# Optimization experiments

Hardware: AMD Instinct MI355X
Metric: run time of the kernel (lower is better)

The kernel has to match this reference:

```python
import jax, jax.numpy as jnp
import numpy as np

B, H, W, C, A, K = 1_000_000, 4, 4, 3, 4, 20
# slicing offsets (w_offset, h_offset) exactly as in the torch code
OFFSETS = [(0, 1), (2, 1), (1, 0), (1, 2)]


def setup_inputs() -> dict:
    key = jax.random.key(0)
    k0, k1, k2, k3, k4, k5 = jax.random.split(key, 6)
    obs = jax.random.normal(k0, (B, H, W, C), dtype=jnp.float32)
    # channel 1 encodes the agent position: exactly one nonzero per sample
    pos = jax.random.randint(k1, (B,), 0, H * W)
    ch1 = jnp.zeros((B, H * W), jnp.float32).at[jnp.arange(B), pos].set(1.0)
    obs = obs.at[..., 1].set(ch1.reshape(B, H, W)).reshape(B, H * W * C)
    s = 0.05  # keep |p| < 1 mostly so the K-step VI recursion stays bounded
    return {
        'obs': obs,
        'Phi_W': jax.random.normal(k2, (48, 48), jnp.float32) * s,
        'Phi_b': jax.random.normal(k3, (48,), jnp.float32) * s,
        'Logit_W': jax.random.normal(k4, (A, 36), jnp.float32) * s,
        'Logit_b': jax.random.normal(k5, (A,), jnp.float32) * s,
    }


def _pad2(x):
    # zero-pad last two spatial dims of (B, H, W) by 1
    return jnp.pad(x, ((0, 0), (1, 1), (1, 1)))


def reference(obs, Phi_W, Phi_b, Logit_W, Logit_b):
    out = (obs @ Phi_W.T + Phi_b).reshape(B, H, W, C)
    rin, rout, p = out[..., 0], out[..., 1], out[..., 2]
    rin_pad = _pad2(rin)  # (B, 6, 6)

    def step(v, _):
        vp = _pad2(v)  # (B, 6, 6)
        for wo, ho in OFFSETS:
            nv = p * vp[:, ho:ho + H, wo:wo + W] + rin_pad[:, ho:ho + H, wo:wo + W] - rout
            v = jnp.maximum(v, nv)
        return v, None

    V, _ = jax.lax.scan(step, jnp.zeros((B, H, W), jnp.float32), None, length=K)

    # agent position: first nonzero of channel 1 (row-major), default (1,1) -> flat 5
    obs4 = obs.reshape(B, H, W, C)
    nz = (obs4[..., 1] != 0).reshape(B, H * W)
    idx = jnp.where(nz.any(axis=1), jnp.argmax(nz, axis=1), 5)
    i, j = idx // W, idx % W

    # 3x3 windows around (i, j) in zero-padded state / value maps
    obs_pad = jnp.pad(obs4, ((0, 0), (1, 1), (1, 1), (0, 0)))  # (B, 6, 6, 3)
    V_pad = _pad2(V)                                            # (B, 6, 6)
    d = jnp.arange(3)
    rows = i[:, None, None] + d[:, None]   # (B, 3, 1)
    cols = j[:, None, None] + d[None, :]   # (B, 1, 3)
    bb = jnp.arange(B)[:, None, None]
    sub_state = obs_pad[bb, rows, cols]    # (B, 3, 3, 3)
    sub_v = V_pad[bb, rows, cols]          # (B, 3, 3)

    logit_in = jnp.concatenate([sub_state.reshape(B, 27), sub_v.reshape(B, 9)], axis=1)
    logit = logit_in @ Logit_W.T + Logit_b  # (B, A)
    return logit
```

## Files before the change

### kernel.cpp

```cpp
#include <hip/hip_runtime.h>

#define BT 256
#define WREG 13312

typedef __attribute__((ext_vector_type(8))) short short8;
typedef __attribute__((ext_vector_type(4))) float f32x4;
typedef __attribute__((ext_vector_type(4))) unsigned int u32x4;
typedef _Float16 h2 __attribute__((ext_vector_type(2)));

__device__ inline unsigned cvtpkbf(float a, float b) {
    unsigned d;
    asm("v_cvt_pk_bf16_f32 %0, %1, %2" : "=v"(d) : "v"(a), "v"(b));
    return d;
}
__device__ inline float b2f(short s) {
    unsigned u = ((unsigned)(unsigned short)s) << 16;
    return __builtin_bit_cast(float, u);
}
__device__ inline unsigned pkrtz(float a, float b) {
    unsigned d;
    asm("v_cvt_pkrtz_f16_f32 %0, %1, %2" : "=v"(d) : "v"(a), "v"(b));
    return d;
}
__device__ inline unsigned pkfma(unsigned a, unsigned b, unsigned c) {
    unsigned d;
    asm("v_pk_fma_f16 %0, %1, %2, %3" : "=v"(d) : "v"(a), "v"(b), "v"(c));
    return d;
}
__device__ inline unsigned pkmax(unsigned a, unsigned b) {
    unsigned d;
    asm("v_pk_max_f16 %0, %1, %2" : "=v"(d) : "v"(a), "v"(b));
    return d;
}

__global__ __launch_bounds__(BT, 3) void vin_kernel(
    const float* __restrict__ obs,
    const float* __restrict__ PhiW,
    const float* __restrict__ Phib,
    const float* __restrict__ LW,
    const float* __restrict__ Lb,
    float* __restrict__ out, int Btot)
{
    __shared__ __align__(16) char smem[4 * WREG];
    const int tid  = threadIdx.x;
    const int lane = tid & 63;
    const int wid  = tid >> 6;
    const int b    = blockIdx.x * BT + tid;
    if (b >= Btot) return;

    char* wbase = smem + wid * WREG;
    const int jn = lane & 15;
    const int g  = lane >> 4;

    float o[48];
    {
        const float4* g4 = reinterpret_cast<const float4*>(obs + (size_t)b * 48);
        #pragma unroll
        for (int q = 0; q < 12; ++q) {
            float4 t = g4[q];
            o[4*q+0] = t.x; o[4*q+1] = t.y; o[4*q+2] = t.z; o[4*q+3] = t.w;
        }
    }

    float ssum = o[1], sidx = 0.0f;
    #pragma unroll
    for (int k = 1; k < 16; ++k) {
        ssum += o[k*3 + 1];
        sidx = fmaf(o[k*3 + 1], (float)k, sidx);
    }
    const int idx = (ssum != 0.0f) ? (int)(sidx + 0.5f) : 5;
    const int ai = idx >> 2;
    const int aj = idx & 3;

    short8 bfrag[3][2];
    #pragma unroll
    for (int n = 0; n < 3; ++n) {
        const float* wrow = PhiW + (16*n + jn) * 48;
        float4 q0 = *reinterpret_cast<const float4*>(wrow + 8*g);
        float4 q1 = *reinterpret_cast<const float4*>(wrow + 8*g + 4);
        u32x4 t0;
        t0[0] = cvtpkbf(q0.x, q0.y); t0[1] = cvtpkbf(q0.z, q0.w);
        t0[2] = cvtpkbf(q1.x, q1.y); t0[3] = cvtpkbf(q1.z, q1.w);
        bfrag[n][0] = __builtin_bit_cast(short8, t0);
        u32x4 tz = {0u, 0u, 0u, 0u};
        if (g < 2) {
            float4 q2 = *reinterpret_cast<const float4*>(wrow + 32 + 8*g);
            float4 q3 = *reinterpret_cast<const float4*>(wrow + 36 + 8*g);
            tz[0] = cvtpkbf(q2.x, q2.y); tz[1] = cvtpkbf(q2.z, q2.w);
            tz[2] = cvtpkbf(q3.x, q3.y); tz[3] = cvtpkbf(q3.z, q3.w);
        }
        bfrag[n][1] = __builtin_bit_cast(short8, tz);
    }

    {
        u32x4* arow = reinterpret_cast<u32x4*>(wbase + lane * 144);
        #pragma unroll
        for (int q = 0; q < 6; ++q) {
            u32x4 v;
            #pragma unroll
            for (int e = 0; e < 4; ++e)
                v[e] = cvtpkbf(o[q*8 + 2*e], o[q*8 + 2*e + 1]);
            arow[q] = v;
        }
        u32x4 z = {0u, 0u, 0u, 0u};
        arow[6] = z; arow[7] = z;
    }

    float lg0 = Lb[0], lg1 = Lb[1], lg2 = Lb[2], lg3 = Lb[3];
    {
        const short* myobs = reinterpret_cast<const short*>(wbase + lane * 144);
        #pragma unroll
        for (int dh = 0; dh < 3; ++dh)
            #pragma unroll
            for (int dw = 0; dw < 3; ++dw) {
                int r = ai + dh - 1, c = aj + dw - 1;
                bool ok = ((unsigned)r < 4u) && ((unsigned)c < 4u);
                int ba = ok ? (r*4 + c) * 3 : 48;
                float s0 = b2f(myobs[ba+0]);
                float s1 = b2f(myobs[ba+1]);
                float s2 = b2f(myobs[ba+2]);
                int f = (dh*3 + dw) * 3;
                lg0 = fmaf(s0, LW[0*36+f], fmaf(s1, LW[0*36+f+1], fmaf(s2, LW[0*36+f+2], lg0)));
                lg1 = fmaf(s0, LW[1*36+f], fmaf(s1, LW[1*36+f+1], fmaf(s2, LW[1*36+f+2], lg1)));
                lg2 = fmaf(s0, LW[2*36+f], fmaf(s1, LW[2*36+f+1], fmaf(s2, LW[2*36+f+2], lg2)));
                lg3 = fmaf(s0, LW[3*36+f], fmaf(s1, LW[3*36+f+1], fmaf(s2, LW[3*36+f+2], lg3)));
            }
    }

    short8 afrag[4][2];
    #pragma unroll
    for (int m = 0; m < 4; ++m) {
        const char* rp = wbase + (m*16 + jn) * 144;
        afrag[m][0] = *reinterpret_cast<const short8*>(rp + 16*g);
        afrag[m][1] = *reinterpret_cast<const short8*>(rp + 64 + 16*g);
    }

    f32x4 acc[4][3];
    {
        float b0 = Phib[jn], b1 = Phib[16 + jn], b2 = Phib[32 + jn];
        #pragma unroll
        for (int m = 0; m < 4; ++m) {
            acc[m][0] = (f32x4){b0, b0, b0, b0};
            acc[m][1] = (f32x4){b1, b1, b1, b1};
            acc[m][2] = (f32x4){b2, b2, b2, b2};
        }
    }
    #pragma unroll
    for (int n = 0; n < 3; ++n)
        #pragma unroll
        for (int m = 0; m < 4; ++m) {
            acc[m][n] = __builtin_amdgcn_mfma_f32_16x16x32_bf16(afrag[m][0], bfrag[n][0], acc[m][n], 0, 0, 0);
            acc[m][n] = __builtin_amdgcn_mfma_f32_16x16x32_bf16(afrag[m][1], bfrag[n][1], acc[m][n], 0, 0, 0);
        }

    asm volatile("s_waitcnt lgkmcnt(0)" ::: "memory");
    __builtin_amdgcn_sched_barrier(0);

    #pragma unroll
    for (int m = 0; m < 4; ++m)
        #pragma unroll
        for (int n = 0; n < 3; ++n)
            #pragma unroll
            for (int r = 0; r < 4; ++r) {
                int row = m*16 + g*4 + r;
                reinterpret_cast<float*>(wbase + row * 208)[n*16 + jn] = acc[m][n][r];
            }

    asm volatile("s_waitcnt lgkmcnt(0)" ::: "memory");
    __builtin_amdgcn_sched_barrier(0);

    float ro[48];
    {
        const char* myrow = wbase + lane * 208;
        #pragma unroll
        for (int q = 0; q < 12; ++q) {
            f32x4 t = *reinterpret_cast<const f32x4*>(myrow + q * 16);
            ro[4*q+0] = t[0]; ro[4*q+1] = t[1]; ro[4*q+2] = t[2]; ro[4*q+3] = t[3];
        }
    }

    float pcf[16], aLf[16], aRf[16], aUf[16], aDf[16];
    #pragma unroll
    for (int h = 0; h < 4; ++h)
        #pragma unroll
        for (int w = 0; w < 4; ++w) {
            int cl = h*4 + w;
            float rout = ro[cl*3 + 1];
            pcf[cl] = ro[cl*3 + 2];
            aLf[cl] = ((w > 0) ? ro[(cl-1)*3] : 0.0f) - rout;
            aRf[cl] = ((w < 3) ? ro[(cl+1)*3] : 0.0f) - rout;
            aUf[cl] = ((h > 0) ? ro[(cl-4)*3] : 0.0f) - rout;
            aDf[cl] = ((h < 3) ? ro[(cl+4)*3] : 0.0f) - rout;
        }

    unsigned p2[4][2], aL2[4][2], aR2[4][2], aU2[4][2], aD2[4][2];
    #pragma unroll
    for (int h = 0; h < 4; ++h)
        #pragma unroll
        for (int j = 0; j < 2; ++j) {
            int c0 = h*4 + j, c1 = h*4 + j + 2;
            p2[h][j]  = pkrtz(pcf[c0], pcf[c1]);
            aL2[h][j] = pkrtz(aLf[c0], aLf[c1]);
            aR2[h][j] = pkrtz(aRf[c0], aRf[c1]);
            aU2[h][j] = pkrtz(aUf[c0], aUf[c1]);
            aD2[h][j] = pkrtz(aDf[c0], aDf[c1]);
        }

    unsigned Vp[4][2];
    #pragma unroll
    for (int h = 0; h < 4; ++h) { Vp[h][0] = 0u; Vp[h][1] = 0u; }

    #pragma unroll 1
    for (int s = 0; s < 20; ++s) {
        unsigned shl[4], shr[4], Vn[4][2];
        #pragma unroll
        for (int h = 0; h < 4; ++h) {
            shl[h] = Vp[h][1] << 16;
            shr[h] = Vp[h][0] >> 16;
        }
        #pragma unroll
        for (int h = 0; h < 4; ++h)
            #pragma unroll
            for (int j = 0; j < 2; ++j) {
                unsigned vL = j ? Vp[h][0] : shl[h];
                unsigned vR = j ? shr[h] : Vp[h][1];
                unsigned tU = (h > 0) ? pkfma(p2[h][j], Vp[h-1][j], aU2[h][j]) : aU2[h][j];
                unsigned tD = (h < 3) ? pkfma(p2[h][j], Vp[h+1][j], aD2[h][j]) : aD2[h][j];
                unsigned m1 = pkmax(Vp[h][j], pkfma(p2[h][j], vL, aL2[h][j]));
                unsigned m2 = pkmax(pkfma(p2[h][j], vR, aR2[h][j]), tU);
                Vn[h][j] = pkmax(pkmax(m1, m2), tD);
            }
        #pragma unroll
        for (int h = 0; h < 4; ++h) { Vp[h][0] = Vn[h][0]; Vp[h][1] = Vn[h][1]; }
    }

    {
        char* myrow = wbase + lane * 208;
        #pragma unroll
        for (int h = 0; h < 4; ++h) {
            h2 a = __builtin_bit_cast(h2, Vp[h][0]);
            h2 c = __builtin_bit_cast(h2, Vp[h][1]);
            *reinterpret_cast<f32x4*>(myrow + h * 16) =
                (f32x4){(float)a[0], (float)c[0], (float)a[1], (float)c[1]};
        }
        *reinterpret_cast<float*>(myrow + 64) = 0.0f;
    }
    asm volatile("s_waitcnt lgkmcnt(0)" ::: "memory");
    __builtin_amdgcn_sched_barrier(0);
    {
        const float* myv = reinterpret_cast<const float*>(wbase + lane * 208);
        #pragma unroll
        for (int dh = 0; dh < 3; ++dh)
            #pragma unroll
            for (int dw = 0; dw < 3; ++dw) {
                int r = ai + dh - 1, c = aj + dw - 1;
                bool ok = ((unsigned)r < 4u) && ((unsigned)c < 4u);
                int ba = ok ? (r*4 + c) : 16;
                float v = myv[ba];
                int f = 27 + dh*3 + dw;
                lg0 = fmaf(v, LW[0*36+f], lg0);
                lg1 = fmaf(v, LW[1*36+f], lg1);
                lg2 = fmaf(v, LW[2*36+f], lg2);
                lg3 = fmaf(v, LW[3*36+f], lg3);
            }
    }

    reinterpret_cast<float4*>(out)[b] = make_float4(lg0, lg1, lg2, lg3);
}

extern "C" void kernel_launch(void* const* d_in, const int* in_sizes, int n_in,
                              void* d_out, int out_size, void* d_ws, size_t ws_size,
                              hipStream_t stream) {
    const float* obs  = (const float*)d_in[0];
    const float* PhiW = (const float*)d_in[1];
    const float* Phib = (const float*)d_in[2];
    const float* LW   = (const float*)d_in[3];
    const float* Lb   = (const float*)d_in[4];
    float* out = (float*)d_out;

    const int Btot = in_sizes[0] / 48;
    const int grid = (Btot + BT - 1) / BT;
    hipLaunchKernelGGL(vin_kernel, dim3(grid), dim3(BT), 0, stream,
                       obs, PhiW, Phib, LW, Lb, out, Btot);
}
```

Before: 70.41 us.

## Stage MFMA output transpose per column tile to shrink LDS and raise occupancy

The per-wave LDS transpose of the 64x48 Phi output now runs in three 16-column passes with a 144-byte row stride instead of one 208-byte pass, which cuts per-wave LDS from 13 KB to 9 KB. Launch bounds go from 3 to 4 blocks per CU to match. Pre-iteration neighbour terms are now built with packed f16 subtracts after packing rin/rout, rather than in fp32 before packing. The aim is higher occupancy and lower register pressure, paid for with extra LDS waits and barriers. The packed-f16 subtraction also changes rounding slightly.

```diff
diff --git a/kernel.cpp b/kernel.cpp
--- a/kernel.cpp
+++ b/kernel.cpp
@@ -1,7 +1,7 @@
 #include <hip/hip_runtime.h>
 
 #define BT 256
-#define WREG 13312
+#define WREG 9216
 
 typedef __attribute__((ext_vector_type(8))) short short8;
 typedef __attribute__((ext_vector_type(4))) float f32x4;
@@ -32,8 +32,18 @@
     asm("v_pk_max_f16 %0, %1, %2" : "=v"(d) : "v"(a), "v"(b));
     return d;
 }
-
-__global__ __launch_bounds__(BT, 3) void vin_kernel(
+__device__ inline unsigned pksub(unsigned a, unsigned b) {
+    unsigned d;
+    asm("v_pk_add_f16 %0, %1, %2 neg_lo:[0,1] neg_hi:[0,1]" : "=v"(d) : "v"(a), "v"(b));
+    return d;
+}
+__device__ inline unsigned pkneg(unsigned b) {
+    unsigned d;
+    asm("v_pk_add_f16 %0, 0, %1 neg_lo:[0,1] neg_hi:[0,1]" : "=v"(d) : "v"(b));
+    return d;
+}
+
+__global__ __launch_bounds__(BT, 4) void vin_kernel(
     const float* __restrict__ obs,
     const float* __restrict__ PhiW,
     const float* __restrict__ Phib,
@@ -156,55 +166,58 @@
     asm volatile("s_waitcnt lgkmcnt(0)" ::: "memory");
     __builtin_amdgcn_sched_barrier(0);
 
-    #pragma unroll
-    for (int m = 0; m < 4; ++m)
-        #pragma unroll
-        for (int n = 0; n < 3; ++n)
+    float rinf[16], routf[16], pcf[16];
+    #pragma unroll
+    for (int n = 0; n < 3; ++n) {
+        #pragma unroll
+        for (int m = 0; m < 4; ++m)
             #pragma unroll
             for (int r = 0; r < 4; ++r) {
                 int row = m*16 + g*4 + r;
-                reinterpret_cast<float*>(wbase + row * 208)[n*16 + jn] = acc[m][n][r];
-            }
-
-    asm volatile("s_waitcnt lgkmcnt(0)" ::: "memory");
-    __builtin_amdgcn_sched_barrier(0);
-
-    float ro[48];
-    {
-        const char* myrow = wbase + lane * 208;
-        #pragma unroll
-        for (int q = 0; q < 12; ++q) {
+                reinterpret_cast<float*>(wbase + row * 144)[jn] = acc[m][n][r];
+            }
+        asm volatile("s_waitcnt lgkmcnt(0)" ::: "memory");
+        __builtin_amdgcn_sched_barrier(0);
+        const char* myrow = wbase + lane * 144;
+        #pragma unroll
+        for (int q = 0; q < 4; ++q) {
             f32x4 t = *reinterpret_cast<const f32x4*>(myrow + q * 16);
-            ro[4*q+0] = t[0]; ro[4*q+1] = t[1]; ro[4*q+2] = t[2]; ro[4*q+3] = t[3];
-        }
-    }
-
-    float pcf[16], aLf[16], aRf[16], aUf[16], aDf[16];
+            #pragma unroll
+            for (int e = 0; e < 4; ++e) {
+                int c = 16*n + 4*q + e;
+                int cell = c / 3, ch = c - 3*cell;
+                if (ch == 0)      rinf[cell]  = t[e];
+                else if (ch == 1) routf[cell] = t[e];
+                else              pcf[cell]   = t[e];
+            }
+        }
+        asm volatile("s_waitcnt lgkmcnt(0)" ::: "memory");
+        __builtin_amdgcn_sched_barrier(0);
+    }
+
+    unsigned rinp[4][2], routp[4][2], pp[4][2];
     #pragma unroll
     for (int h = 0; h < 4; ++h)
         #pragma unroll
-        for (int w = 0; w < 4; ++w) {
-            int cl = h*4 + w;
-            float rout = ro[cl*3 + 1];
-            pcf[cl] = ro[cl*3 + 2];
-            aLf[cl] = ((w > 0) ? ro[(cl-1)*3] : 0.0f) - rout;
-            aRf[cl] = ((w < 3) ? ro[(cl+1)*3] : 0.0f) - rout;
-            aUf[cl] = ((h > 0) ? ro[(cl-4)*3] : 0.0f) - rout;
-            aDf[cl] = ((h < 3) ? ro[(cl+4)*3] : 0.0f) - rout;
-        }
-
-    unsigned p2[4][2], aL2[4][2], aR2[4][2], aU2[4][2], aD2[4][2];
-    #pragma unroll
-    for (int h = 0; h < 4; ++h)
-        #pragma unroll
         for (int j = 0; j < 2; ++j) {
-            int c0 = h*4 + j, c1 = h*4 + j + 2;
-            p2[h][j]  = pkrtz(pcf[c0], pcf[c1]);
-            aL2[h][j] = pkrtz(aLf[c0], aLf[c1]);
-            aR2[h][j] = pkrtz(aRf[c0], aRf[c1]);
-            aU2[h][j] = pkrtz(aUf[c0], aUf[c1]);
-            aD2[h][j] = pkrtz(aDf[c0], aDf[c1]);
-        }
+            int c0 = 4*h + j, c1 = 4*h + j + 2;
+            rinp[h][j]  = pkrtz(rinf[c0], rinf[c1]);
+            routp[h][j] = pkrtz(routf[c0], routf[c1]);
+            pp[h][j]    = pkrtz(pcf[c0], pcf[c1]);
+        }
+    unsigned aL2[4][2], aR2[4][2], aU2[4][2], aD2[4][2];
+    #pragma unroll
+    for (int h = 0; h < 4; ++h) {
+        aL2[h][0] = pksub(rinp[h][1] << 16, routp[h][0]);
+        aL2[h][1] = pksub(rinp[h][0], routp[h][1]);
+        aR2[h][0] = pksub(rinp[h][1], routp[h][0]);
+        aR2[h][1] = pksub(rinp[h][0] >> 16, routp[h][1]);
+        #pragma unroll
+        for (int j = 0; j < 2; ++j) {
+            aU2[h][j] = (h > 0) ? pksub(rinp[h-1][j], routp[h][j]) : pkneg(routp[0][j]);
+            aD2[h][j] = (h < 3) ? pksub(rinp[h+1][j], routp[h][j]) : pkneg(routp[3][j]);
+        }
+    }
 
     unsigned Vp[4][2];
     #pragma unroll
@@ -224,10 +237,10 @@
             for (int j = 0; j < 2; ++j) {
                 unsigned vL = j ? Vp[h][0] : shl[h];
                 unsigned vR = j ? shr[h] : Vp[h][1];
-                unsigned tU = (h > 0) ? pkfma(p2[h][j], Vp[h-1][j], aU2[h][j]) : aU2[h][j];
-                unsigned tD = (h < 3) ? pkfma(p2[h][j], Vp[h+1][j], aD2[h][j]) : aD2[h][j];
-                unsigned m1 = pkmax(Vp[h][j], pkfma(p2[h][j], vL, aL2[h][j]));
-                unsigned m2 = pkmax(pkfma(p2[h][j], vR, aR2[h][j]), tU);
+                unsigned tU = (h > 0) ? pkfma(pp[h][j], Vp[h-1][j], aU2[h][j]) : aU2[h][j];
+                unsigned tD = (h < 3) ? pkfma(pp[h][j], Vp[h+1][j], aD2[h][j]) : aD2[h][j];
+                unsigned m1 = pkmax(Vp[h][j], pkfma(pp[h][j], vL, aL2[h][j]));
+                unsigned m2 = pkmax(pkfma(pp[h][j], vR, aR2[h][j]), tU);
                 Vn[h][j] = pkmax(pkmax(m1, m2), tD);
             }
         #pragma unroll
@@ -235,7 +248,7 @@
     }
 
     {
-        char* myrow = wbase + lane * 208;
+        char* myrow = wbase + lane * 144;
         #pragma unroll
         for (int h = 0; h < 4; ++h) {
             h2 a = __builtin_bit_cast(h2, Vp[h][0]);
@@ -248,7 +261,7 @@
     asm volatile("s_waitcnt lgkmcnt(0)" ::: "memory");
     __builtin_amdgcn_sched_barrier(0);
     {
-        const float* myv = reinterpret_cast<const float*>(wbase + lane * 208);
+        const float* myv = reinterpret_cast<const float*>(wbase + lane * 144);
         #pragma unroll
         for (int dh = 0; dh < 3; ++dh)
             #pragma unroll
```

Measured after the change: 70.73 us. About the same (+0.5%).
